# Performance work log

Hardware: AMD Instinct MI355X
Metric: run time of the kernel (lower is better)

## Reference

```python
import jax, jax.numpy as jnp
import numpy as np

D = 768
NH = 12
HD = D // NH
N_MLP = 3072
LN_EPS = 1e-6


def layer_norm(x, g, b, eps=LN_EPS):
    mu = jnp.mean(x, axis=-1, keepdims=True)
    var = jnp.mean(jnp.square(x - mu), axis=-1, keepdims=True)
    return (x - mu) * jax.lax.rsqrt(var + eps) * g + b


def setup_inputs() -> dict:
    key = jax.random.key(0)
    ks = jax.random.split(key, 6)
    x = jax.random.normal(ks[0], (2, 4096, D), dtype=jnp.float32)
    # torch Linear weights are (out, in); init std=0.02, zero bias
    W_qkv = 0.02 * jax.random.normal(ks[1], (3 * D, D), dtype=jnp.float32)
    b_qkv = jnp.zeros((3 * D,), dtype=jnp.float32)
    W_proj = 0.02 * jax.random.normal(ks[2], (D, D), dtype=jnp.float32)
    b_proj = jnp.zeros((D,), dtype=jnp.float32)
    W1 = 0.02 * jax.random.normal(ks[3], (N_MLP, D), dtype=jnp.float32)
    b1 = jnp.zeros((N_MLP,), dtype=jnp.float32)
    W2 = 0.02 * jax.random.normal(ks[4], (D, N_MLP), dtype=jnp.float32)
    b2 = jnp.zeros((D,), dtype=jnp.float32)
    g1 = jnp.ones((D,), dtype=jnp.float32)
    beta1 = jnp.zeros((D,), dtype=jnp.float32)
    g2 = jnp.ones((D,), dtype=jnp.float32)
    beta2 = jnp.zeros((D,), dtype=jnp.float32)
    return dict(x=x, W_qkv=W_qkv, b_qkv=b_qkv, W_proj=W_proj, b_proj=b_proj,
                W1=W1, b1=b1, W2=W2, b2=b2,
                g1=g1, beta1=beta1, g2=g2, beta2=beta2)


def reference(x, W_qkv, b_qkv, W_proj, b_proj, W1, b1, W2, b2, g1, beta1, g2, beta2):
    B, T, d = x.shape
    scale = HD ** (-0.5)
    # --- attention branch (pre-norm) ---
    h = layer_norm(x, g1, beta1)
    qkv = h @ W_qkv.T + b_qkv                      # [B,T,3d]
    qkv = qkv.reshape(B, T, 3, NH, HD)
    q, k, v = qkv[:, :, 0], qkv[:, :, 1], qkv[:, :, 2]  # [B,T,NH,HD]
    logits = jnp.einsum('bthc,bshc->bhts', q, k) * scale
    attn = jax.nn.softmax(logits, axis=-1)
    out = jnp.einsum('bhts,bshc->bthc', attn, v).reshape(B, T, d)
    out = out @ W_proj.T + b_proj
    x = x + out
    # --- MLP branch (pre-norm) ---
    h = layer_norm(x, g2, beta2)
    h = jax.nn.gelu(h @ W1.T + b1, approximate=False)
    h = h @ W2.T + b2
    return x + h
```

## Files before the change

kernel.cpp:

```cpp
#include <hip/hip_runtime.h>
#include <cmath>

typedef __attribute__((ext_vector_type(4))) float f32x4;
typedef __attribute__((ext_vector_type(16))) float f32x16;
typedef __attribute__((ext_vector_type(8))) __bf16 bf16x8;
typedef __attribute__((ext_vector_type(8))) unsigned short u16x8;
typedef __attribute__((ext_vector_type(4))) unsigned short u16x4;
typedef __attribute__((ext_vector_type(2))) unsigned int u32x2;
typedef __attribute__((ext_vector_type(4))) unsigned int u32x4;

#define DEV __device__ __forceinline__

DEV unsigned short f2b(float v) {
  __bf16 b = (__bf16)v;
  return __builtin_bit_cast(unsigned short, b);
}

DEV unsigned int cvtpk(float lo, float hi) {
  unsigned int r;
  asm("v_cvt_pk_bf16_f32 %0, %1, %2" : "=v"(r) : "v"(lo), "v"(hi));
  return r;
}

DEV float exp2a(float x) {
  float r;
  asm("v_exp_f32 %0, %1" : "=v"(r) : "v"(x));
  return r;
}

DEV void swap32(unsigned int& x, unsigned int& y) {
  asm("v_permlane32_swap_b32 %0, %1" : "+v"(x), "+v"(y));
}

DEV u32x2 tr_b16(const unsigned short* p) {
  u32x2 r;
  asm volatile("ds_read_b64_tr_b16 %0, %1"
               : "=v"(r)
               : "v"((unsigned int)(unsigned long long)p)
               : "memory");
  return r;
}

DEV void gll16(const void* g, const void* l) {
  __builtin_amdgcn_global_load_lds(
      (const __attribute__((address_space(1))) unsigned int*)(unsigned long long)g,
      (__attribute__((address_space(3))) unsigned int*)(unsigned int)(unsigned long long)l,
      16, 0, 0);
}

DEV float bflo(unsigned int u) { return __builtin_bit_cast(float, u << 16); }
DEV float bfhi(unsigned int u) { return __builtin_bit_cast(float, u & 0xFFFF0000u); }

__global__ void k_cvt_all(const float* __restrict__ s0, const float* __restrict__ s1,
                          const float* __restrict__ s2, const float* __restrict__ s3,
                          unsigned short* __restrict__ dst) {
  int i = blockIdx.x * blockDim.x + threadIdx.x;
  const float* s;
  unsigned short* d;
  if (i < 442368) {
    s = s0 + (size_t)i * 4;
    d = dst + (size_t)i * 4;
  } else if (i < 589824) {
    int j = i - 442368;
    s = s1 + (size_t)j * 4;
    d = dst + 1769472 + (size_t)j * 4;
  } else if (i < 1179648) {
    int j = i - 589824;
    s = s2 + (size_t)j * 4;
    d = dst + 2359296 + (size_t)j * 4;
  } else {
    int j = i - 1179648;
    s = s3 + (size_t)j * 4;
    d = dst + 4718592 + (size_t)j * 4;
  }
  float4 v = *(const float4*)s;
  u16x4 o = {f2b(v.x), f2b(v.y), f2b(v.z), f2b(v.w)};
  *(u16x4*)d = o;
}

__global__ void k_ln(const float* __restrict__ x, const float* __restrict__ g,
                     const float* __restrict__ be, unsigned short* __restrict__ out) {
  int row = blockIdx.x;
  int l = threadIdx.x;
  const float* xr = x + (size_t)row * 768;
  float4 v[3];
  float s = 0.f, sq = 0.f;
#pragma unroll
  for (int j = 0; j < 3; ++j) {
    v[j] = ((const float4*)xr)[l + 64 * j];
    s += v[j].x + v[j].y + v[j].z + v[j].w;
    sq += v[j].x * v[j].x + v[j].y * v[j].y + v[j].z * v[j].z + v[j].w * v[j].w;
  }
#pragma unroll
  for (int m = 1; m < 64; m <<= 1) {
    s += __shfl_xor(s, m);
    sq += __shfl_xor(sq, m);
  }
  float mu = s * (1.f / 768.f);
  float var = sq * (1.f / 768.f) - mu * mu;
  float rs = rsqrtf(var + 1e-6f);
  unsigned short* orow = out + (size_t)row * 768;
#pragma unroll
  for (int j = 0; j < 3; ++j) {
    int c4 = l + 64 * j;
    float4 gv = ((const float4*)g)[c4];
    float4 bv = ((const float4*)be)[c4];
    u16x4 o = {f2b((v[j].x - mu) * rs * gv.x + bv.x),
               f2b((v[j].y - mu) * rs * gv.y + bv.y),
               f2b((v[j].z - mu) * rs * gv.z + bv.z),
               f2b((v[j].w - mu) * rs * gv.w + bv.w)};
    *(u16x4*)(orow + c4 * 4) = o;
  }
}

template <int MODE, int BM>
__global__ __launch_bounds__(256, 2) void k_gemm(
    const unsigned short* __restrict__ A, const unsigned short* __restrict__ Bw,
    const float* __restrict__ bias, const float* __restrict__ res,
    void* __restrict__ outp, int N, int K) {
  __shared__ unsigned short As[2][BM * 64];
  __shared__ unsigned short Bs[2][128 * 64];
  constexpr int MR = BM / 32;
  constexpr int AI = BM / 32;
  constexpr int LPT = AI + 4;
  const int tid = threadIdx.x;
  const int w = tid >> 6, l = tid & 63;
  const int wr = w >> 1, wc = w & 1;
  const int lr = l & 15, lg = l >> 4;
  const int nwg = gridDim.x * gridDim.y;
  const int bid = blockIdx.y * gridDim.x + blockIdx.x;
  const int swz = (bid & 7) * (nwg >> 3) + (bid >> 3);
  const int bx = swz % gridDim.x, by = swz / gridDim.x;
  const int brow = by * BM, bcol = bx * 128;

  auto stage = [&](int buf, int kt) {
#pragma unroll
    for (int i = 0; i < AI; ++i) {
      int c = i * 256 + tid;
      int row = c >> 3, cg = (c & 7) ^ (row & 7);
      gll16(A + (size_t)(brow + row) * K + kt + cg * 8,
            (const char*)&As[buf][0] + (i * 256 + (w << 6)) * 16);
    }
#pragma unroll
    for (int i = 0; i < 4; ++i) {
      int c = i * 256 + tid;
      int row = c >> 3, cg = (c & 7) ^ (row & 7);
      gll16(Bw + (size_t)(bcol + row) * K + kt + cg * 8,
            (const char*)&Bs[buf][0] + (i * 256 + (w << 6)) * 16);
    }
  };

  stage(0, 0);
  if (64 < K) stage(1, 64);
  f32x4 acc[MR][4] = {};
  for (int kt = 0, t = 0; kt < K; kt += 64, ++t) {
    const int cur = t & 1;
    if (kt + 64 < K) {
      if constexpr (LPT == 8)
        asm volatile("s_waitcnt vmcnt(8)" ::: "memory");
      else
        asm volatile("s_waitcnt vmcnt(6)" ::: "memory");
    } else {
      asm volatile("s_waitcnt vmcnt(0)" ::: "memory");
    }
    __builtin_amdgcn_s_barrier();
    __builtin_amdgcn_sched_barrier(0);
    bf16x8 af[MR][2], bfr[4][2];
#pragma unroll
    for (int m = 0; m < MR; ++m) {
      int row = wr * (BM / 2) + m * 16 + lr;
#pragma unroll
      for (int s = 0; s < 2; ++s)
        af[m][s] = *(const bf16x8*)&As[cur][row * 64 + (((s * 4 + lg) ^ (row & 7)) << 3)];
    }
#pragma unroll
    for (int n = 0; n < 4; ++n) {
      int row = wc * 64 + n * 16 + lr;
#pragma unroll
      for (int s = 0; s < 2; ++s)
        bfr[n][s] = *(const bf16x8*)&Bs[cur][row * 64 + (((s * 4 + lg) ^ (row & 7)) << 3)];
    }
    asm volatile("s_waitcnt lgkmcnt(0)" ::: "memory");
    __builtin_amdgcn_sched_barrier(0);
    __builtin_amdgcn_s_barrier();
    if (kt + 128 < K) stage(cur, kt + 128);
    __builtin_amdgcn_s_setprio(1);
#pragma unroll
    for (int s = 0; s < 2; ++s)
#pragma unroll
      for (int m = 0; m < MR; ++m)
#pragma unroll
        for (int n = 0; n < 4; ++n)
          acc[m][n] =
              __builtin_amdgcn_mfma_f32_16x16x32_bf16(af[m][s], bfr[n][s], acc[m][n], 0, 0, 0);
    __builtin_amdgcn_s_setprio(0);
  }
#pragma unroll
  for (int n = 0; n < 4; ++n) {
    int col = bcol + wc * 64 + n * 16 + lr;
    float bv = bias[col];
#pragma unroll
    for (int m = 0; m < MR; ++m) {
      int row0 = brow + wr * (BM / 2) + m * 16 + lg * 4;
#pragma unroll
      for (int r = 0; r < 4; ++r) {
        size_t idx = (size_t)(row0 + r) * N + col;
        float v = acc[m][n][r] + bv;
        if (MODE == 0) {
          ((unsigned short*)outp)[idx] = f2b(v);
        } else if (MODE == 1) {
          ((float*)outp)[idx] = v + res[idx];
        } else if (MODE == 2) {
          ((unsigned short*)outp)[idx] = f2b(0.5f * v * (1.f + erff(v * 0.70710678f)));
        } else {
          ((float*)outp)[idx] = v + res[idx];
        }
      }
    }
  }
}

__global__ __launch_bounds__(256, 4) void k_attn(const unsigned short* __restrict__ qkv,
                                                 u32x4* __restrict__ Opk,
                                                 float* __restrict__ ml) {
  __shared__ unsigned short Ks[2][64 * 64];
  __shared__ unsigned short Vs[2][4 * 64 * 16];
  const int tid = threadIdx.x;
  const int w = tid >> 6, l = tid & 63;
  const int lq = l & 31, hi = l >> 5;
  const int p = blockIdx.x;
  const int linear = (p & 7) * 192 + (p >> 3);
  const int bh = linear >> 6, rem = linear & 63;
  const int qt = rem >> 1, half = rem & 1;
  const int b = bh / 12, h = bh % 12;
  const size_t base = (size_t)b * 4096 * 2304;
  const int qbase = qt * 128 + w * 32;
  const int kv0 = half * 2048;

  const float SC = 0.18033688f;
  bf16x8 qb[4];
#pragma unroll
  for (int s = 0; s < 4; ++s) {
    u16x8 raw = *(const u16x8*)(qkv + base + (size_t)(qbase + lq) * 2304 + h * 64 +
                                s * 16 + hi * 8);
    u32x4 pk;
#pragma unroll
    for (int d = 0; d < 4; ++d) {
      float f0 = __builtin_bit_cast(float, (unsigned int)raw[2 * d] << 16) * SC;
      float f1 = __builtin_bit_cast(float, (unsigned int)raw[2 * d + 1] << 16) * SC;
      pk[d] = cvtpk(f0, f1);
    }
    qb[s] = __builtin_bit_cast(bf16x8, pk);
  }

  const unsigned short* pK = qkv + base + (size_t)(kv0 + 16 * w + (l >> 3)) * 2304 + 768 +
                             h * 64 + (((l & 7) ^ ((l >> 3) & 7)) << 3);
  const unsigned short* pV = qkv + base + (size_t)(kv0 + (l >> 1)) * 2304 + 1536 + h * 64 +
                             w * 16 + ((l & 1) << 3);
  const size_t STEP = (size_t)64 * 2304;

  {
    const char* dK = (const char*)&Ks[0][0] + w * 2048;
    const char* dV = (const char*)&Vs[0][0] + w * 2048;
    gll16(pK, dK);
    gll16(pK + 8 * 2304, dK + 1024);
    gll16(pV, dV);
    gll16(pV + 32 * 2304, dV + 1024);
    pK += STEP;
    pV += STEP;
  }

  f32x16 O[2] = {};
  float lrun = 0.f;

  int it = 0;
  for (int t = 0; t < 32; ++t, it ^= 1) {
    asm volatile("s_waitcnt vmcnt(0)" ::: "memory");
    __syncthreads();
    if (t < 31) {
      const char* dK = (const char*)&Ks[it ^ 1][0] + w * 2048;
      const char* dV = (const char*)&Vs[it ^ 1][0] + w * 2048;
      gll16(pK, dK);
      gll16(pK + 8 * 2304, dK + 1024);
      gll16(pV, dV);
      gll16(pV + 32 * 2304, dV + 1024);
      pK += STEP;
      pV += STEP;
    }

    f32x16 st[2] = {{0}, {0}};
    __builtin_amdgcn_s_setprio(1);
#pragma unroll
    for (int kt = 0; kt < 2; ++kt) {
      int key = kt * 32 + lq;
#pragma unroll
      for (int s = 0; s < 4; ++s) {
        bf16x8 ka =
            *(const bf16x8*)&Ks[it][key * 64 + ((s * 16 + hi * 8) ^ ((key & 7) << 3))];
        st[kt] = __builtin_amdgcn_mfma_f32_32x32x16_bf16(ka, qb[s], st[kt], 0, 0, 0);
      }
    }
    __builtin_amdgcn_s_setprio(0);

    float s0 = 0.f, s1 = 0.f, s2 = 0.f, s3 = 0.f;
#pragma unroll
    for (int kt = 0; kt < 2; ++kt) {
#pragma unroll
      for (int r = 0; r < 16; r += 4) {
        float p0 = exp2a(st[kt][r + 0]);
        float p1 = exp2a(st[kt][r + 1]);
        float p2 = exp2a(st[kt][r + 2]);
        float p3 = exp2a(st[kt][r + 3]);
        st[kt][r + 0] = p0;
        st[kt][r + 1] = p1;
        st[kt][r + 2] = p2;
        st[kt][r + 3] = p3;
        s0 += p0;
        s1 += p1;
        s2 += p2;
        s3 += p3;
      }
    }
    float ssum = (s0 + s1) + (s2 + s3);
    lrun += ssum + __shfl_xor(ssum, 32);

    u32x4 pf[4];
#pragma unroll
    for (int kt = 0; kt < 2; ++kt)
#pragma unroll
      for (int h2 = 0; h2 < 2; ++h2) {
        int r0 = h2 * 8;
        unsigned int a0 = cvtpk(st[kt][r0 + 0], st[kt][r0 + 1]);
        unsigned int a1 = cvtpk(st[kt][r0 + 2], st[kt][r0 + 3]);
        unsigned int b0 = cvtpk(st[kt][r0 + 4], st[kt][r0 + 5]);
        unsigned int b1 = cvtpk(st[kt][r0 + 6], st[kt][r0 + 7]);
        swap32(a0, b0);
        swap32(a1, b1);
        pf[kt * 2 + h2] = u32x4{a0, a1, b0, b1};
      }

#pragma unroll
    for (int hb = 0; hb < 2; ++hb) {
      u32x2 vt[4][2];
      const unsigned short* vbase = &Vs[it][(hb * 2 + (lq >> 4)) * 1024 + (lq & 15)];
#pragma unroll
      for (int s = 0; s < 4; ++s)
#pragma unroll
        for (int t2 = 0; t2 < 2; ++t2)
          vt[s][t2] = tr_b16(vbase + ((s * 16 + hi * 8 + t2 * 4) << 4));
      asm volatile("s_waitcnt lgkmcnt(0)" ::: "memory");
      __builtin_amdgcn_sched_barrier(0);
      __builtin_amdgcn_s_setprio(1);
#pragma unroll
      for (int s = 0; s < 4; ++s) {
        u32x4 vv = {vt[s][0].x, vt[s][0].y, vt[s][1].x, vt[s][1].y};
        O[hb] = __builtin_amdgcn_mfma_f32_32x32x16_bf16(
            __builtin_bit_cast(bf16x8, vv), __builtin_bit_cast(bf16x8, pf[s]), O[hb], 0, 0, 0);
      }
      __builtin_amdgcn_s_setprio(0);
    }
  }

  if (hi == 0) ml[(linear * 4 + w) * 32 + lq] = lrun;
#pragma unroll
  for (int hb = 0; hb < 2; ++hb)
#pragma unroll
    for (int v = 0; v < 2; ++v) {
      u32x4 pkv = {cvtpk(O[hb][8 * v + 0], O[hb][8 * v + 1]),
                   cvtpk(O[hb][8 * v + 2], O[hb][8 * v + 3]),
                   cvtpk(O[hb][8 * v + 4], O[hb][8 * v + 5]),
                   cvtpk(O[hb][8 * v + 6], O[hb][8 * v + 7])};
      Opk[((linear * 4 + w) * 4 + hb * 2 + v) * 64 + l] = pkv;
    }
}

__global__ __launch_bounds__(256) void k_merge(const u32x4* __restrict__ Opk,
                                               const float* __restrict__ ml,
                                               unsigned short* __restrict__ out) {
  const int g = blockIdx.x;
  const int bh = g >> 5, qt = g & 31;
  const int b = bh / 12, h = bh % 12;
  const int tid = threadIdx.x;
  const int w = tid >> 6, l = tid & 63;
  const int lq = l & 31, hi = l >> 5;
  const int bidA = bh * 64 + qt * 2;
  const int bidB = bidA + 1;
  float l0 = ml[(bidA * 4 + w) * 32 + lq];
  float l1 = ml[(bidB * 4 + w) * 32 + lq];
  float rl = 1.f / (l0 + l1);
  const int t = qt * 128 + w * 32 + lq;
  unsigned short* orow = out + (size_t)(b * 4096 + t) * 768 + h * 64;
#pragma unroll
  for (int hb = 0; hb < 2; ++hb)
#pragma unroll
    for (int v = 0; v < 2; ++v) {
      u32x4 va = Opk[((bidA * 4 + w) * 4 + hb * 2 + v) * 64 + l];
      u32x4 vb = Opk[((bidB * 4 + w) * 4 + hb * 2 + v) * 64 + l];
      unsigned int dw[4];
#pragma unroll
      for (int d = 0; d < 4; ++d) {
        float lo = (bflo(va[d]) + bflo(vb[d])) * rl;
        float hi2 = (bfhi(va[d]) + bfhi(vb[d])) * rl;
        dw[d] = cvtpk(lo, hi2);
      }
      *(u32x2*)(orow + hb * 32 + 8 * (2 * v) + 4 * hi) = u32x2{dw[0], dw[1]};
      *(u32x2*)(orow + hb * 32 + 8 * (2 * v + 1) + 4 * hi) = u32x2{dw[2], dw[3]};
    }
}

extern "C" void kernel_launch(void* const* d_in, const int* in_sizes, int n_in,
                              void* d_out, int out_size, void* d_ws, size_t ws_size,
                              hipStream_t stream) {
  const float* x = (const float*)d_in[0];
  const float* Wqkv = (const float*)d_in[1];
  const float* bqkv = (const float*)d_in[2];
  const float* Wproj = (const float*)d_in[3];
  const float* bproj = (const float*)d_in[4];
  const float* W1 = (const float*)d_in[5];
  const float* b1 = (const float*)d_in[6];
  const float* W2 = (const float*)d_in[7];
  const float* b2 = (const float*)d_in[8];
  const float* g1 = (const float*)d_in[9];
  const float* be1 = (const float*)d_in[10];
  const float* g2 = (const float*)d_in[11];
  const float* be2 = (const float*)d_in[12];

  char* ws = (char*)d_ws;
  unsigned short* wqkv = (unsigned short*)(ws + 0);
  unsigned short* wproj = (unsigned short*)(ws + 3538944);
  unsigned short* ww1 = (unsigned short*)(ws + 4718592);
  unsigned short* ww2 = (unsigned short*)(ws + 9437184);
  unsigned short* h1 = (unsigned short*)(ws + 14155776);
  unsigned short* qkvb = (unsigned short*)(ws + 26738688);
  unsigned short* attno = (unsigned short*)(ws + 64487424);
  float* x1 = (float*)(ws + 77070336);
  unsigned short* h2 = (unsigned short*)(ws + 102236160);
  unsigned short* m1 = (unsigned short*)(ws + 114819072);
  u32x4* Opk = (u32x4*)m1;
  float* mlbuf = (float*)h1;

  k_cvt_all<<<6912, 256, 0, stream>>>(Wqkv, Wproj, W1, W2, wqkv);

  k_ln<<<8192, 64, 0, stream>>>(x, g1, be1, h1);
  k_gemm<0, 128><<<dim3(18, 64), 256, 0, stream>>>(h1, wqkv, bqkv, nullptr, qkvb, 2304, 768);
  k_attn<<<1536, 256, 0, stream>>>(qkvb, Opk, mlbuf);
  k_merge<<<768, 256, 0, stream>>>(Opk, mlbuf, attno);
  k_gemm<1, 128><<<dim3(6, 64), 256, 0, stream>>>(attno, wproj, bproj, x, x1, 768, 768);
  k_ln<<<8192, 64, 0, stream>>>(x1, g2, be2, h2);
  k_gemm<2, 128><<<dim3(24, 64), 256, 0, stream>>>(h2, ww1, b1, nullptr, m1, 3072, 768);
  k_gemm<3, 128><<<dim3(6, 64), 256, 0, stream>>>(m1, ww2, b2, x1, (float*)d_out, 768, 3072);
}
```

Baseline: 334.0 us.

## Fuse LN with weight conversion, halve GEMM K-tile, compute softmax sums via MFMA

Merges the first layer norm and the fp32-to-bf16 weight conversion into one launch, and packs four LN rows per 256-thread block. Cuts the GEMM K tile from 64 to 32, which halves LDS use, possibly for occupancy, but doubles the number of barriers per K. In attention, the per-row softmax denominator now comes from an extra MFMA against a ones vector instead of scalar adds and a cross-lane shuffle. Together these target launch overhead, VALU work and LDS pressure, at the cost of more sync steps in the GEMM loop and a denominator summed from bf16-rounded probabilities.

```diff
diff --git a/kernel.cpp b/kernel.cpp
--- a/kernel.cpp
+++ b/kernel.cpp
@@ -51,38 +51,8 @@
 DEV float bflo(unsigned int u) { return __builtin_bit_cast(float, u << 16); }
 DEV float bfhi(unsigned int u) { return __builtin_bit_cast(float, u & 0xFFFF0000u); }
 
-__global__ void k_cvt_all(const float* __restrict__ s0, const float* __restrict__ s1,
-                          const float* __restrict__ s2, const float* __restrict__ s3,
-                          unsigned short* __restrict__ dst) {
-  int i = blockIdx.x * blockDim.x + threadIdx.x;
-  const float* s;
-  unsigned short* d;
-  if (i < 442368) {
-    s = s0 + (size_t)i * 4;
-    d = dst + (size_t)i * 4;
-  } else if (i < 589824) {
-    int j = i - 442368;
-    s = s1 + (size_t)j * 4;
-    d = dst + 1769472 + (size_t)j * 4;
-  } else if (i < 1179648) {
-    int j = i - 589824;
-    s = s2 + (size_t)j * 4;
-    d = dst + 2359296 + (size_t)j * 4;
-  } else {
-    int j = i - 1179648;
-    s = s3 + (size_t)j * 4;
-    d = dst + 4718592 + (size_t)j * 4;
-  }
-  float4 v = *(const float4*)s;
-  u16x4 o = {f2b(v.x), f2b(v.y), f2b(v.z), f2b(v.w)};
-  *(u16x4*)d = o;
-}
-
-__global__ void k_ln(const float* __restrict__ x, const float* __restrict__ g,
-                     const float* __restrict__ be, unsigned short* __restrict__ out) {
-  int row = blockIdx.x;
-  int l = threadIdx.x;
-  const float* xr = x + (size_t)row * 768;
+DEV void ln_row(const float* __restrict__ xr, const float* __restrict__ g,
+                const float* __restrict__ be, unsigned short* __restrict__ orow, int l) {
   float4 v[3];
   float s = 0.f, sq = 0.f;
 #pragma unroll
@@ -99,7 +69,6 @@
   float mu = s * (1.f / 768.f);
   float var = sq * (1.f / 768.f) - mu * mu;
   float rs = rsqrtf(var + 1e-6f);
-  unsigned short* orow = out + (size_t)row * 768;
 #pragma unroll
   for (int j = 0; j < 3; ++j) {
     int c4 = l + 64 * j;
@@ -113,16 +82,58 @@
   }
 }
 
+__global__ void k_ln(const float* __restrict__ x, const float* __restrict__ g,
+                     const float* __restrict__ be, unsigned short* __restrict__ out) {
+  int row = blockIdx.x * 4 + (threadIdx.x >> 6);
+  int l = threadIdx.x & 63;
+  ln_row(x + (size_t)row * 768, g, be, out + (size_t)row * 768, l);
+}
+
+__global__ void k_pre(const float* __restrict__ x, const float* __restrict__ g,
+                      const float* __restrict__ be, unsigned short* __restrict__ h1,
+                      const float* __restrict__ s0, const float* __restrict__ s1,
+                      const float* __restrict__ s2, const float* __restrict__ s3,
+                      unsigned short* __restrict__ wdst) {
+  int bid = blockIdx.x;
+  if (bid < 2048) {
+    int row = bid * 4 + (threadIdx.x >> 6);
+    int l = threadIdx.x & 63;
+    ln_row(x + (size_t)row * 768, g, be, h1 + (size_t)row * 768, l);
+    return;
+  }
+  int i = (bid - 2048) * 256 + threadIdx.x;
+  const float* s;
+  unsigned short* d;
+  if (i < 442368) {
+    s = s0 + (size_t)i * 4;
+    d = wdst + (size_t)i * 4;
+  } else if (i < 589824) {
+    int j = i - 442368;
+    s = s1 + (size_t)j * 4;
+    d = wdst + 1769472 + (size_t)j * 4;
+  } else if (i < 1179648) {
+    int j = i - 589824;
+    s = s2 + (size_t)j * 4;
+    d = wdst + 2359296 + (size_t)j * 4;
+  } else {
+    int j = i - 1179648;
+    s = s3 + (size_t)j * 4;
+    d = wdst + 4718592 + (size_t)j * 4;
+  }
+  float4 v = *(const float4*)s;
+  u16x4 o = {f2b(v.x), f2b(v.y), f2b(v.z), f2b(v.w)};
+  *(u16x4*)d = o;
+}
+
 template <int MODE, int BM>
 __global__ __launch_bounds__(256, 2) void k_gemm(
     const unsigned short* __restrict__ A, const unsigned short* __restrict__ Bw,
     const float* __restrict__ bias, const float* __restrict__ res,
     void* __restrict__ outp, int N, int K) {
-  __shared__ unsigned short As[2][BM * 64];
-  __shared__ unsigned short Bs[2][128 * 64];
+  __shared__ unsigned short As[2][BM * 32];
+  __shared__ unsigned short Bs[2][128 * 32];
   constexpr int MR = BM / 32;
-  constexpr int AI = BM / 32;
-  constexpr int LPT = AI + 4;
+  constexpr int AI = BM / 64;
   const int tid = threadIdx.x;
   const int w = tid >> 6, l = tid & 63;
   const int wr = w >> 1, wc = w & 1;
@@ -137,62 +148,51 @@
 #pragma unroll
     for (int i = 0; i < AI; ++i) {
       int c = i * 256 + tid;
-      int row = c >> 3, cg = (c & 7) ^ (row & 7);
+      int row = c >> 2, cg = (c & 3) ^ (row & 3);
       gll16(A + (size_t)(brow + row) * K + kt + cg * 8,
             (const char*)&As[buf][0] + (i * 256 + (w << 6)) * 16);
     }
 #pragma unroll
-    for (int i = 0; i < 4; ++i) {
+    for (int i = 0; i < 2; ++i) {
       int c = i * 256 + tid;
-      int row = c >> 3, cg = (c & 7) ^ (row & 7);
+      int row = c >> 2, cg = (c & 3) ^ (row & 3);
       gll16(Bw + (size_t)(bcol + row) * K + kt + cg * 8,
             (const char*)&Bs[buf][0] + (i * 256 + (w << 6)) * 16);
     }
   };
 
   stage(0, 0);
-  if (64 < K) stage(1, 64);
+  if (32 < K) stage(1, 32);
   f32x4 acc[MR][4] = {};
-  for (int kt = 0, t = 0; kt < K; kt += 64, ++t) {
+  for (int kt = 0, t = 0; kt < K; kt += 32, ++t) {
     const int cur = t & 1;
-    if (kt + 64 < K) {
-      if constexpr (LPT == 8)
-        asm volatile("s_waitcnt vmcnt(8)" ::: "memory");
-      else
-        asm volatile("s_waitcnt vmcnt(6)" ::: "memory");
-    } else {
+    if (kt + 32 < K)
+      asm volatile("s_waitcnt vmcnt(4)" ::: "memory");
+    else
       asm volatile("s_waitcnt vmcnt(0)" ::: "memory");
-    }
     __builtin_amdgcn_s_barrier();
     __builtin_amdgcn_sched_barrier(0);
-    bf16x8 af[MR][2], bfr[4][2];
+    bf16x8 af[MR], bfr[4];
 #pragma unroll
     for (int m = 0; m < MR; ++m) {
       int row = wr * (BM / 2) + m * 16 + lr;
-#pragma unroll
-      for (int s = 0; s < 2; ++s)
-        af[m][s] = *(const bf16x8*)&As[cur][row * 64 + (((s * 4 + lg) ^ (row & 7)) << 3)];
+      af[m] = *(const bf16x8*)&As[cur][row * 32 + ((lg ^ (row & 3)) << 3)];
     }
 #pragma unroll
     for (int n = 0; n < 4; ++n) {
       int row = wc * 64 + n * 16 + lr;
-#pragma unroll
-      for (int s = 0; s < 2; ++s)
-        bfr[n][s] = *(const bf16x8*)&Bs[cur][row * 64 + (((s * 4 + lg) ^ (row & 7)) << 3)];
+      bfr[n] = *(const bf16x8*)&Bs[cur][row * 32 + ((lg ^ (row & 3)) << 3)];
     }
     asm volatile("s_waitcnt lgkmcnt(0)" ::: "memory");
     __builtin_amdgcn_sched_barrier(0);
     __builtin_amdgcn_s_barrier();
-    if (kt + 128 < K) stage(cur, kt + 128);
+    if (kt + 64 < K) stage(cur, kt + 64);
     __builtin_amdgcn_s_setprio(1);
 #pragma unroll
-    for (int s = 0; s < 2; ++s)
-#pragma unroll
-      for (int m = 0; m < MR; ++m)
-#pragma unroll
-        for (int n = 0; n < 4; ++n)
-          acc[m][n] =
-              __builtin_amdgcn_mfma_f32_16x16x32_bf16(af[m][s], bfr[n][s], acc[m][n], 0, 0, 0);
+    for (int m = 0; m < MR; ++m)
+#pragma unroll
+      for (int n = 0; n < 4; ++n)
+        acc[m][n] = __builtin_amdgcn_mfma_f32_16x16x32_bf16(af[m], bfr[n], acc[m][n], 0, 0, 0);
     __builtin_amdgcn_s_setprio(0);
   }
 #pragma unroll
@@ -271,7 +271,10 @@
   }
 
   f32x16 O[2] = {};
-  float lrun = 0.f;
+  f32x16 lacc = {};
+  const unsigned int ONE2 = 0x3F803F80u;
+  const u32x4 ones4 = {ONE2, ONE2, ONE2, ONE2};
+  const bf16x8 ones = __builtin_bit_cast(bf16x8, ones4);
 
   int it = 0;
   for (int t = 0; t < 32; ++t, it ^= 1) {
@@ -302,27 +305,10 @@
     }
     __builtin_amdgcn_s_setprio(0);
 
-    float s0 = 0.f, s1 = 0.f, s2 = 0.f, s3 = 0.f;
-#pragma unroll
-    for (int kt = 0; kt < 2; ++kt) {
-#pragma unroll
-      for (int r = 0; r < 16; r += 4) {
-        float p0 = exp2a(st[kt][r + 0]);
-        float p1 = exp2a(st[kt][r + 1]);
-        float p2 = exp2a(st[kt][r + 2]);
-        float p3 = exp2a(st[kt][r + 3]);
-        st[kt][r + 0] = p0;
-        st[kt][r + 1] = p1;
-        st[kt][r + 2] = p2;
-        st[kt][r + 3] = p3;
-        s0 += p0;
-        s1 += p1;
-        s2 += p2;
-        s3 += p3;
-      }
-    }
-    float ssum = (s0 + s1) + (s2 + s3);
-    lrun += ssum + __shfl_xor(ssum, 32);
+#pragma unroll
+    for (int kt = 0; kt < 2; ++kt)
+#pragma unroll
+      for (int r = 0; r < 16; ++r) st[kt][r] = exp2a(st[kt][r]);
 
     u32x4 pf[4];
 #pragma unroll
@@ -340,6 +326,11 @@
       }
 
 #pragma unroll
+    for (int s = 0; s < 4; ++s)
+      lacc = __builtin_amdgcn_mfma_f32_32x32x16_bf16(
+          ones, __builtin_bit_cast(bf16x8, pf[s]), lacc, 0, 0, 0);
+
+#pragma unroll
     for (int hb = 0; hb < 2; ++hb) {
       u32x2 vt[4][2];
       const unsigned short* vbase = &Vs[it][(hb * 2 + (lq >> 4)) * 1024 + (lq & 15)];
@@ -361,7 +352,7 @@
     }
   }
 
-  if (hi == 0) ml[(linear * 4 + w) * 32 + lq] = lrun;
+  if (hi == 0) ml[(linear * 4 + w) * 32 + lq] = lacc[0];
 #pragma unroll
   for (int hb = 0; hb < 2; ++hb)
 #pragma unroll
@@ -439,14 +430,13 @@
   u32x4* Opk = (u32x4*)m1;
   float* mlbuf = (float*)h1;
 
-  k_cvt_all<<<6912, 256, 0, stream>>>(Wqkv, Wproj, W1, W2, wqkv);
-
-  k_ln<<<8192, 64, 0, stream>>>(x, g1, be1, h1);
+  k_pre<<<8960, 256, 0, stream>>>(x, g1, be1, h1, Wqkv, Wproj, W1, W2, wqkv);
+
   k_gemm<0, 128><<<dim3(18, 64), 256, 0, stream>>>(h1, wqkv, bqkv, nullptr, qkvb, 2304, 768);
   k_attn<<<1536, 256, 0, stream>>>(qkvb, Opk, mlbuf);
   k_merge<<<768, 256, 0, stream>>>(Opk, mlbuf, attno);
   k_gemm<1, 128><<<dim3(6, 64), 256, 0, stream>>>(attno, wproj, bproj, x, x1, 768, 768);
-  k_ln<<<8192, 64, 0, stream>>>(x1, g2, be2, h2);
+  k_ln<<<2048, 256, 0, stream>>>(x1, g2, be2, h2);
   k_gemm<2, 128><<<dim3(24, 64), 256, 0, stream>>>(h2, ww1, b1, nullptr, m1, 3072, 768);
   k_gemm<3, 128><<<dim3(6, 64), 256, 0, stream>>>(m1, ww2, b2, x1, (float*)d_out, 768, 3072);
 }
```

Result: slower. 342.4 us, median of 2 (+2.5%).

## Switch GEMM to 32x32x16 MFMA, fuse LN with weight cast, batch LN rows

Applied to the files above, without the earlier changes.

The GEMM kernel now uses 32x32x16 bf16 MFMA tiles with 16-float accumulators instead of 16x16x32, which halves the fragment count per wave and increases operand reuse per LDS read. The first LayerNorm and the weight fp32-to-bf16 conversion are merged into one launch to save a kernel launch and let the two run concurrently. LayerNorm also now processes four rows per 256-thread block instead of one row per 64-thread block. Risks include a different LDS bank access pattern for the new fragment reads and a strided epilogue store layout.

```diff
diff --git a/kernel.cpp b/kernel.cpp
--- a/kernel.cpp
+++ b/kernel.cpp
@@ -51,38 +51,8 @@
 DEV float bflo(unsigned int u) { return __builtin_bit_cast(float, u << 16); }
 DEV float bfhi(unsigned int u) { return __builtin_bit_cast(float, u & 0xFFFF0000u); }
 
-__global__ void k_cvt_all(const float* __restrict__ s0, const float* __restrict__ s1,
-                          const float* __restrict__ s2, const float* __restrict__ s3,
-                          unsigned short* __restrict__ dst) {
-  int i = blockIdx.x * blockDim.x + threadIdx.x;
-  const float* s;
-  unsigned short* d;
-  if (i < 442368) {
-    s = s0 + (size_t)i * 4;
-    d = dst + (size_t)i * 4;
-  } else if (i < 589824) {
-    int j = i - 442368;
-    s = s1 + (size_t)j * 4;
-    d = dst + 1769472 + (size_t)j * 4;
-  } else if (i < 1179648) {
-    int j = i - 589824;
-    s = s2 + (size_t)j * 4;
-    d = dst + 2359296 + (size_t)j * 4;
-  } else {
-    int j = i - 1179648;
-    s = s3 + (size_t)j * 4;
-    d = dst + 4718592 + (size_t)j * 4;
-  }
-  float4 v = *(const float4*)s;
-  u16x4 o = {f2b(v.x), f2b(v.y), f2b(v.z), f2b(v.w)};
-  *(u16x4*)d = o;
-}
-
-__global__ void k_ln(const float* __restrict__ x, const float* __restrict__ g,
-                     const float* __restrict__ be, unsigned short* __restrict__ out) {
-  int row = blockIdx.x;
-  int l = threadIdx.x;
-  const float* xr = x + (size_t)row * 768;
+DEV void ln_row(const float* __restrict__ xr, const float* __restrict__ g,
+                const float* __restrict__ be, unsigned short* __restrict__ orow, int l) {
   float4 v[3];
   float s = 0.f, sq = 0.f;
 #pragma unroll
@@ -99,7 +69,6 @@
   float mu = s * (1.f / 768.f);
   float var = sq * (1.f / 768.f) - mu * mu;
   float rs = rsqrtf(var + 1e-6f);
-  unsigned short* orow = out + (size_t)row * 768;
 #pragma unroll
   for (int j = 0; j < 3; ++j) {
     int c4 = l + 64 * j;
@@ -113,6 +82,49 @@
   }
 }
 
+__global__ void k_ln(const float* __restrict__ x, const float* __restrict__ g,
+                     const float* __restrict__ be, unsigned short* __restrict__ out) {
+  int row = blockIdx.x * 4 + (threadIdx.x >> 6);
+  int l = threadIdx.x & 63;
+  ln_row(x + (size_t)row * 768, g, be, out + (size_t)row * 768, l);
+}
+
+__global__ void k_pre(const float* __restrict__ x, const float* __restrict__ g,
+                      const float* __restrict__ be, unsigned short* __restrict__ h1,
+                      const float* __restrict__ s0, const float* __restrict__ s1,
+                      const float* __restrict__ s2, const float* __restrict__ s3,
+                      unsigned short* __restrict__ wdst) {
+  int bid = blockIdx.x;
+  if (bid < 2048) {
+    int row = bid * 4 + (threadIdx.x >> 6);
+    int l = threadIdx.x & 63;
+    ln_row(x + (size_t)row * 768, g, be, h1 + (size_t)row * 768, l);
+    return;
+  }
+  int i = (bid - 2048) * 256 + threadIdx.x;
+  const float* s;
+  unsigned short* d;
+  if (i < 442368) {
+    s = s0 + (size_t)i * 4;
+    d = wdst + (size_t)i * 4;
+  } else if (i < 589824) {
+    int j = i - 442368;
+    s = s1 + (size_t)j * 4;
+    d = wdst + 1769472 + (size_t)j * 4;
+  } else if (i < 1179648) {
+    int j = i - 589824;
+    s = s2 + (size_t)j * 4;
+    d = wdst + 2359296 + (size_t)j * 4;
+  } else {
+    int j = i - 1179648;
+    s = s3 + (size_t)j * 4;
+    d = wdst + 4718592 + (size_t)j * 4;
+  }
+  float4 v = *(const float4*)s;
+  u16x4 o = {f2b(v.x), f2b(v.y), f2b(v.z), f2b(v.w)};
+  *(u16x4*)d = o;
+}
+
 template <int MODE, int BM>
 __global__ __launch_bounds__(256, 2) void k_gemm(
     const unsigned short* __restrict__ A, const unsigned short* __restrict__ Bw,
@@ -120,13 +132,13 @@
     void* __restrict__ outp, int N, int K) {
   __shared__ unsigned short As[2][BM * 64];
   __shared__ unsigned short Bs[2][128 * 64];
-  constexpr int MR = BM / 32;
+  constexpr int MR = BM / 64;
   constexpr int AI = BM / 32;
   constexpr int LPT = AI + 4;
   const int tid = threadIdx.x;
   const int w = tid >> 6, l = tid & 63;
   const int wr = w >> 1, wc = w & 1;
-  const int lr = l & 15, lg = l >> 4;
+  const int l31 = l & 31, khalf = l >> 5;
   const int nwg = gridDim.x * gridDim.y;
   const int bid = blockIdx.y * gridDim.x + blockIdx.x;
   const int swz = (bid & 7) * (nwg >> 3) + (bid >> 3);
@@ -152,7 +164,7 @@
 
   stage(0, 0);
   if (64 < K) stage(1, 64);
-  f32x4 acc[MR][4] = {};
+  f32x16 acc[MR][2] = {};
   for (int kt = 0, t = 0; kt < K; kt += 64, ++t) {
     const int cur = t & 1;
     if (kt + 64 < K) {
@@ -165,20 +177,22 @@
     }
     __builtin_amdgcn_s_barrier();
     __builtin_amdgcn_sched_barrier(0);
-    bf16x8 af[MR][2], bfr[4][2];
+    bf16x8 af[MR][4], bfr[2][4];
 #pragma unroll
     for (int m = 0; m < MR; ++m) {
-      int row = wr * (BM / 2) + m * 16 + lr;
-#pragma unroll
-      for (int s = 0; s < 2; ++s)
-        af[m][s] = *(const bf16x8*)&As[cur][row * 64 + (((s * 4 + lg) ^ (row & 7)) << 3)];
-    }
-#pragma unroll
-    for (int n = 0; n < 4; ++n) {
-      int row = wc * 64 + n * 16 + lr;
-#pragma unroll
-      for (int s = 0; s < 2; ++s)
-        bfr[n][s] = *(const bf16x8*)&Bs[cur][row * 64 + (((s * 4 + lg) ^ (row & 7)) << 3)];
+      int row = wr * (BM / 2) + m * 32 + l31;
+#pragma unroll
+      for (int s = 0; s < 4; ++s)
+        af[m][s] =
+            *(const bf16x8*)&As[cur][row * 64 + (((s * 2 + khalf) ^ (row & 7)) << 3)];
+    }
+#pragma unroll
+    for (int n = 0; n < 2; ++n) {
+      int row = wc * 64 + n * 32 + l31;
+#pragma unroll
+      for (int s = 0; s < 4; ++s)
+        bfr[n][s] =
+            *(const bf16x8*)&Bs[cur][row * 64 + (((s * 2 + khalf) ^ (row & 7)) << 3)];
     }
     asm volatile("s_waitcnt lgkmcnt(0)" ::: "memory");
     __builtin_amdgcn_sched_barrier(0);
@@ -186,25 +200,26 @@
     if (kt + 128 < K) stage(cur, kt + 128);
     __builtin_amdgcn_s_setprio(1);
 #pragma unroll
-    for (int s = 0; s < 2; ++s)
+    for (int s = 0; s < 4; ++s)
 #pragma unroll
       for (int m = 0; m < MR; ++m)
 #pragma unroll
-        for (int n = 0; n < 4; ++n)
-          acc[m][n] =
-              __builtin_amdgcn_mfma_f32_16x16x32_bf16(af[m][s], bfr[n][s], acc[m][n], 0, 0, 0);
+        for (int n = 0; n < 2; ++n)
+          acc[m][n] = __builtin_amdgcn_mfma_f32_32x32x16_bf16(af[m][s], bfr[n][s],
+                                                              acc[m][n], 0, 0, 0);
     __builtin_amdgcn_s_setprio(0);
   }
 #pragma unroll
-  for (int n = 0; n < 4; ++n) {
-    int col = bcol + wc * 64 + n * 16 + lr;
+  for (int n = 0; n < 2; ++n) {
+    int col = bcol + wc * 64 + n * 32 + l31;
     float bv = bias[col];
 #pragma unroll
     for (int m = 0; m < MR; ++m) {
-      int row0 = brow + wr * (BM / 2) + m * 16 + lg * 4;
-#pragma unroll
-      for (int r = 0; r < 4; ++r) {
-        size_t idx = (size_t)(row0 + r) * N + col;
+      int row0 = brow + wr * (BM / 2) + m * 32 + 4 * khalf;
+#pragma unroll
+      for (int r = 0; r < 16; ++r) {
+        int row = row0 + (r & 3) + 8 * (r >> 2);
+        size_t idx = (size_t)row * N + col;
         float v = acc[m][n][r] + bv;
         if (MODE == 0) {
           ((unsigned short*)outp)[idx] = f2b(v);
@@ -439,14 +454,13 @@
   u32x4* Opk = (u32x4*)m1;
   float* mlbuf = (float*)h1;
 
-  k_cvt_all<<<6912, 256, 0, stream>>>(Wqkv, Wproj, W1, W2, wqkv);
-
-  k_ln<<<8192, 64, 0, stream>>>(x, g1, be1, h1);
+  k_pre<<<8960, 256, 0, stream>>>(x, g1, be1, h1, Wqkv, Wproj, W1, W2, wqkv);
+
   k_gemm<0, 128><<<dim3(18, 64), 256, 0, stream>>>(h1, wqkv, bqkv, nullptr, qkvb, 2304, 768);
   k_attn<<<1536, 256, 0, stream>>>(qkvb, Opk, mlbuf);
   k_merge<<<768, 256, 0, stream>>>(Opk, mlbuf, attno);
   k_gemm<1, 128><<<dim3(6, 64), 256, 0, stream>>>(attno, wproj, bproj, x, x1, 768, 768);
-  k_ln<<<8192, 64, 0, stream>>>(x1, g2, be2, h2);
+  k_ln<<<2048, 256, 0, stream>>>(x1, g2, be2, h2);
   k_gemm<2, 128><<<dim3(24, 64), 256, 0, stream>>>(h2, ww1, b1, nullptr, m1, 3072, 768);
   k_gemm<3, 128><<<dim3(6, 64), 256, 0, stream>>>(m1, ww2, b2, x1, (float*)d_out, 768, 3072);
 }
```

Result: slower. 341.3 us (+2.2%).
